# Kernel tuning notes

Hardware: AMD Instinct MI355X
Metric: run time of the kernel (lower is better)

## Reference

```python
import jax, jax.numpy as jnp
import numpy as np

N_NODES = 100000
N_EDGES = 1600000
EMBED_DIM = 64


def setup_inputs() -> dict:
    key = jax.random.key(0)
    k1, k2, k3, k4 = jax.random.split(key, 4)
    ego_embeddings = jax.random.normal(k1, (N_NODES, EMBED_DIM), dtype=jnp.float32)
    adj_values = jax.random.uniform(k2, (N_EDGES,), dtype=jnp.float32)
    adj_rows = jax.random.randint(k3, (N_EDGES,), 0, N_NODES, dtype=jnp.int32)
    adj_cols = jax.random.randint(k4, (N_EDGES,), 0, N_NODES, dtype=jnp.int32)
    return {
        "ego_embeddings": ego_embeddings,
        "adj_values": adj_values,
        "adj_rows": adj_rows,
        "adj_cols": adj_cols,
    }


def reference(ego_embeddings, adj_values, adj_rows, adj_cols):
    # out[r, :] = sum_{e : rows[e]==r} values[e] * ego_embeddings[cols[e], :]
    # == tf.sparse.sparse_dense_matmul(adj, ego_embeddings)
    messages = adj_values[:, None] * ego_embeddings[adj_cols]  # [E, D]
    out = jax.ops.segment_sum(messages, adj_rows, num_segments=N_NODES)  # [N, D]
    return out
```

## Files before the change

### kernel.cpp

```cpp
#include <hip/hip_runtime.h>

#define N_NODES 100000
#define N_EDGES 1600000
#define EMBED_DIM 64

#define RPB 128
#define NBKT ((N_NODES + RPB - 1) / RPB)
#define CAP 2304
#define TILE 4096
#define NTILE ((N_EDGES + TILE - 1) / TILE)
#define OVCAP 8192
#define EPT 3

__global__ __launch_bounds__(1024) void k_binA(const int* __restrict__ rows,
                                               const int* __restrict__ cols,
                                               const float* __restrict__ vals,
                                               int* __restrict__ gcur,
                                               int2* __restrict__ packed,
                                               int* __restrict__ ov_cnt,
                                               int4* __restrict__ ov) {
    __shared__ int hist[NBKT];
    __shared__ int off[NBKT];
    __shared__ int cur[NBKT];
    __shared__ int gbase[NBKT];
    __shared__ int wsum[16];
    __shared__ int stotal;
    __shared__ int2 stage[TILE];
    __shared__ int dg[TILE];
    const int tid = threadIdx.x;
    const int lane = tid & 63;
    const int wid = tid >> 6;
    const int e0 = blockIdx.x * TILE;

    for (int i = tid; i < NBKT; i += 1024) hist[i] = 0;
    __syncthreads();

    const int eb = e0 + 4 * tid;
    int rr0 = -1, rr1 = -1, rr2 = -1, rr3 = -1;
    if (eb + 3 < N_EDGES) {
        int4 r4 = *(const int4*)(rows + eb);
        rr0 = r4.x; rr1 = r4.y; rr2 = r4.z; rr3 = r4.w;
    } else {
        if (eb + 0 < N_EDGES) rr0 = rows[eb + 0];
        if (eb + 1 < N_EDGES) rr1 = rows[eb + 1];
        if (eb + 2 < N_EDGES) rr2 = rows[eb + 2];
        if (eb + 3 < N_EDGES) rr3 = rows[eb + 3];
    }
    if (rr0 >= 0) atomicAdd(&hist[rr0 >> 7], 1);
    if (rr1 >= 0) atomicAdd(&hist[rr1 >> 7], 1);
    if (rr2 >= 0) atomicAdd(&hist[rr2 >> 7], 1);
    if (rr3 >= 0) atomicAdd(&hist[rr3 >> 7], 1);
    __syncthreads();

    int v = (tid < NBKT) ? hist[tid] : 0;
    int incl = v;
    for (int o = 1; o < 64; o <<= 1) {
        int t = __shfl_up(incl, o, 64);
        if (lane >= o) incl += t;
    }
    if (lane == 63) wsum[wid] = incl;
    __syncthreads();
    if (wid == 0 && lane < 16) {
        int s = wsum[lane];
        int si = s;
        for (int o = 1; o < 16; o <<= 1) {
            int t = __shfl_up(si, o, 64);
            if (lane >= o) si += t;
        }
        wsum[lane] = si - s;
        if (lane == 15) stotal = si;
    }
    __syncthreads();
    int excl = incl - v + wsum[wid];
    if (tid < NBKT) { off[tid] = excl; cur[tid] = excl; }

    for (int b = tid; b < NBKT; b += 1024) {
        int c = hist[b];
        gbase[b] = c ? atomicAdd(&gcur[b], c) : 0;
    }
    __syncthreads();

    int cc0 = 0, cc1 = 0, cc2 = 0, cc3 = 0;
    float vv0 = 0.f, vv1 = 0.f, vv2 = 0.f, vv3 = 0.f;
    if (eb + 3 < N_EDGES) {
        int4 c4 = *(const int4*)(cols + eb);
        float4 v4 = *(const float4*)(vals + eb);
        cc0 = c4.x; cc1 = c4.y; cc2 = c4.z; cc3 = c4.w;
        vv0 = v4.x; vv1 = v4.y; vv2 = v4.z; vv3 = v4.w;
    } else {
        if (eb + 0 < N_EDGES) { cc0 = cols[eb + 0]; vv0 = vals[eb + 0]; }
        if (eb + 1 < N_EDGES) { cc1 = cols[eb + 1]; vv1 = vals[eb + 1]; }
        if (eb + 2 < N_EDGES) { cc2 = cols[eb + 2]; vv2 = vals[eb + 2]; }
        if (eb + 3 < N_EDGES) { cc3 = cols[eb + 3]; vv3 = vals[eb + 3]; }
    }
#define PLACE(RR, CC, VV)                                                     \
    if (RR >= 0) {                                                            \
        int b_ = RR >> 7;                                                     \
        int p_ = atomicAdd(&cur[b_], 1);                                      \
        stage[p_] = make_int2(((RR & (RPB - 1)) << 17) | CC,                  \
                              __float_as_int(VV));                            \
        int d_ = gbase[b_] + (p_ - off[b_]);                                  \
        dg[p_] = (d_ < CAP) ? (b_ * CAP + d_) : (0x40000000 | b_);            \
    }
    PLACE(rr0, cc0, vv0)
    PLACE(rr1, cc1, vv1)
    PLACE(rr2, cc2, vv2)
    PLACE(rr3, cc3, vv3)
#undef PLACE
    __syncthreads();

    int total = stotal;
    for (int j = tid; j < total; j += 1024) {
        int d = dg[j];
        int2 ev = stage[j];
        if (d & 0x40000000) {
            int b_ = d & 0xFFFF;
            int ovi = atomicAdd(ov_cnt, 1);
            if (ovi < OVCAP) {
                int r = b_ * RPB + (((unsigned)ev.x) >> 17);
                ov[ovi] = make_int4(r, ev.x & 0x1FFFF, ev.y, 0);
            }
        } else {
            packed[d] = ev;
        }
    }
}

__global__ __launch_bounds__(1024) void k_bg(const float* __restrict__ x,
                                             const int* __restrict__ gcur,
                                             const int2* __restrict__ packed,
                                             const int* __restrict__ ov_cnt,
                                             const int4* __restrict__ ov,
                                             float* __restrict__ out) {
    __shared__ int2 stage[CAP];
    __shared__ int h[RPB];
    __shared__ int ofs[RPB];
    __shared__ int cur[RPB];
    __shared__ int wsum[2];
    const int b = blockIdx.x;
    const int tid = threadIdx.x;
    const int lane = tid & 63;
    const int wid = tid >> 6;
    int n = gcur[b];
    if (n > CAP) n = CAP;
    const int base = b * CAP;

    if (tid < RPB) h[tid] = 0;
    __syncthreads();

    int2 ereg[EPT];
    int lr[EPT];
#pragma unroll
    for (int jj = 0; jj < EPT; ++jj) {
        int j = tid + jj * 1024;
        lr[jj] = -1;
        if (j < n) {
            int2 e = packed[base + j];
            ereg[jj] = e;
            int r = ((unsigned)e.x) >> 17;
            lr[jj] = r;
            atomicAdd(&h[r], 1);
        }
    }
    __syncthreads();

    int hv = (tid < RPB) ? h[tid] : 0;
    int incl = hv;
    for (int o = 1; o < 64; o <<= 1) {
        int t = __shfl_up(incl, o, 64);
        if (lane >= o) incl += t;
    }
    if (tid < RPB && lane == 63) wsum[wid] = incl;
    __syncthreads();
    if (wid == 0 && lane < 2) {
        int s = wsum[lane];
        int si = s;
        {
            int t = __shfl_up(si, 1, 64);
            if (lane >= 1) si += t;
        }
        wsum[lane] = si - s;
    }
    __syncthreads();
    if (tid < RPB) {
        int o2 = incl - hv + wsum[wid];
        ofs[tid] = o2;
        cur[tid] = o2;
    }
    __syncthreads();

#pragma unroll
    for (int jj = 0; jj < EPT; ++jj) {
        if (lr[jj] >= 0) {
            int p = atomicAdd(&cur[lr[jj]], 1);
            stage[p] = ereg[jj];
        }
    }
    __syncthreads();

    const int half = lane >> 5;
    const int hl = lane & 31;
    const float2* __restrict__ x2 = (const float2*)x;
    for (int i = 0; i < 8; ++i) {
        int r = wid * 8 + i;
        int grow = b * RPB + r;
        if (grow >= N_NODES) break;
        int deg = h[r];
        int beg = ofs[r];
        float ax = 0.f, ay = 0.f;
        for (int j0 = 0; j0 < deg; j0 += 16) {
            float pv[8];
            float2 xv[8];
#pragma unroll
            for (int k = 0; k < 8; ++k) {
                int j = j0 + 2 * k + half;
                int2 e = (j < deg) ? stage[beg + j] : make_int2(0, 0);
                pv[k] = __int_as_float(e.y);
                xv[k] = x2[(e.x & 0x1FFFF) * 32 + hl];
            }
#pragma unroll
            for (int k = 0; k < 8; ++k) {
                ax += pv[k] * xv[k].x;
                ay += pv[k] * xv[k].y;
            }
        }
        ax += __shfl_xor(ax, 32);
        ay += __shfl_xor(ay, 32);
        if (half == 0) {
            ((float2*)out)[(size_t)grow * 32 + hl] = make_float2(ax, ay);
        }
    }

    __syncthreads();
    int nov = *ov_cnt;
    if (nov > OVCAP) nov = OVCAP;
    for (int i = wid; i < nov; i += 16) {
        int4 e = ov[i];
        if ((e.x >> 7) == b) {
            atomicAdd(&out[(size_t)e.x * EMBED_DIM + lane],
                      __int_as_float(e.z) * x[(size_t)e.y * EMBED_DIM + lane]);
        }
    }
}

__global__ __launch_bounds__(256) void spmm_scatter_kernel(
    const float* __restrict__ x, const float* __restrict__ vals,
    const int* __restrict__ rows, const int* __restrict__ cols,
    float* __restrict__ out) {
    const int wave_in_block = threadIdx.x >> 6;
    const int lane = threadIdx.x & 63;
    const int e = blockIdx.x * 4 + wave_in_block;
    if (e >= N_EDGES) return;
    const float m = vals[e] * x[cols[e] * EMBED_DIM + lane];
    atomicAdd(&out[rows[e] * EMBED_DIM + lane], m);
}

extern "C" void kernel_launch(void* const* d_in, const int* in_sizes, int n_in,
                              void* d_out, int out_size, void* d_ws, size_t ws_size,
                              hipStream_t stream) {
    const float* x    = (const float*)d_in[0];
    const float* vals = (const float*)d_in[1];
    const int*   rows = (const int*)d_in[2];
    const int*   cols = (const int*)d_in[3];
    float* out = (float*)d_out;

    const size_t packed_b = (size_t)NBKT * CAP * 8;
    const size_t ov_b     = (size_t)OVCAP * 16;
    const size_t need = packed_b + ov_b + ((size_t)NBKT + 1) * 4;
    if (ws_size < need) {
        hipMemsetAsync(out, 0, (size_t)out_size * sizeof(float), stream);
        spmm_scatter_kernel<<<(N_EDGES + 3) / 4, 256, 0, stream>>>(x, vals, rows, cols, out);
        return;
    }

    int2* packed  = (int2*)d_ws;
    int4* ov      = (int4*)((char*)d_ws + packed_b);
    int*  gcur    = (int*)((char*)d_ws + packed_b + ov_b);
    int*  ov_cnt  = gcur + NBKT;

    hipMemsetAsync(gcur, 0, ((size_t)NBKT + 1) * sizeof(int), stream);

    k_binA<<<NTILE, 1024, 0, stream>>>(rows, cols, vals, gcur, packed, ov_cnt, ov);
    k_bg<<<NBKT, 1024, 0, stream>>>(x, gcur, (const int2*)packed, ov_cnt, ov, out);
}
```

Measured before the change: 165.8 us.

## Replace global bucket atomics with per-tile sorted segments gathered by consumer

The binning kernel no longer reserves global slots per bucket with atomics. Each tile now writes its locally bucket-sorted edges contiguously, plus a per-tile offset table. The gather kernel scans each bucket's segment lengths across all tiles and copies those segments into shared memory, spilling overflow to a small shared list. This removes the global atomics, the memset and the scattered global writes, at the cost of serial per-tile segment copies by up to 391 threads and a second random-ish read pattern. It also drops the global overflow buffer scan that every block used to do.

```diff
diff --git a/kernel.cpp b/kernel.cpp
--- a/kernel.cpp
+++ b/kernel.cpp
@@ -6,45 +6,47 @@
 
 #define RPB 128
 #define NBKT ((N_NODES + RPB - 1) / RPB)
-#define CAP 2304
 #define TILE 4096
 #define NTILE ((N_EDGES + TILE - 1) / TILE)
-#define OVCAP 8192
+#define OFFW (NBKT + 1)
+#define SCAP 2816
 #define EPT 3
 
 __global__ __launch_bounds__(1024) void k_binA(const int* __restrict__ rows,
                                                const int* __restrict__ cols,
                                                const float* __restrict__ vals,
-                                               int* __restrict__ gcur,
-                                               int2* __restrict__ packed,
-                                               int* __restrict__ ov_cnt,
-                                               int4* __restrict__ ov) {
+                                               int* __restrict__ off_g,
+                                               int2* __restrict__ packed2) {
     __shared__ int hist[NBKT];
-    __shared__ int off[NBKT];
     __shared__ int cur[NBKT];
-    __shared__ int gbase[NBKT];
     __shared__ int wsum[16];
-    __shared__ int stotal;
     __shared__ int2 stage[TILE];
-    __shared__ int dg[TILE];
     const int tid = threadIdx.x;
     const int lane = tid & 63;
     const int wid = tid >> 6;
-    const int e0 = blockIdx.x * TILE;
+    const int blk = blockIdx.x;
+    const int e0 = blk * TILE;
+    const int total = (blk == NTILE - 1) ? (N_EDGES - e0) : TILE;
 
     for (int i = tid; i < NBKT; i += 1024) hist[i] = 0;
     __syncthreads();
 
     const int eb = e0 + 4 * tid;
     int rr0 = -1, rr1 = -1, rr2 = -1, rr3 = -1;
+    int cc0 = 0, cc1 = 0, cc2 = 0, cc3 = 0;
+    float vv0 = 0.f, vv1 = 0.f, vv2 = 0.f, vv3 = 0.f;
     if (eb + 3 < N_EDGES) {
         int4 r4 = *(const int4*)(rows + eb);
+        int4 c4 = *(const int4*)(cols + eb);
+        float4 v4 = *(const float4*)(vals + eb);
         rr0 = r4.x; rr1 = r4.y; rr2 = r4.z; rr3 = r4.w;
+        cc0 = c4.x; cc1 = c4.y; cc2 = c4.z; cc3 = c4.w;
+        vv0 = v4.x; vv1 = v4.y; vv2 = v4.z; vv3 = v4.w;
     } else {
-        if (eb + 0 < N_EDGES) rr0 = rows[eb + 0];
-        if (eb + 1 < N_EDGES) rr1 = rows[eb + 1];
-        if (eb + 2 < N_EDGES) rr2 = rows[eb + 2];
-        if (eb + 3 < N_EDGES) rr3 = rows[eb + 3];
+        if (eb + 0 < N_EDGES) { rr0 = rows[eb + 0]; cc0 = cols[eb + 0]; vv0 = vals[eb + 0]; }
+        if (eb + 1 < N_EDGES) { rr1 = rows[eb + 1]; cc1 = cols[eb + 1]; vv1 = vals[eb + 1]; }
+        if (eb + 2 < N_EDGES) { rr2 = rows[eb + 2]; cc2 = cols[eb + 2]; vv2 = vals[eb + 2]; }
+        if (eb + 3 < N_EDGES) { rr3 = rows[eb + 3]; cc3 = cols[eb + 3]; vv3 = vals[eb + 3]; }
     }
     if (rr0 >= 0) atomicAdd(&hist[rr0 >> 7], 1);
     if (rr1 >= 0) atomicAdd(&hist[rr1 >> 7], 1);
@@ -68,39 +70,21 @@
             if (lane >= o) si += t;
         }
         wsum[lane] = si - s;
-        if (lane == 15) stotal = si;
     }
     __syncthreads();
     int excl = incl - v + wsum[wid];
-    if (tid < NBKT) { off[tid] = excl; cur[tid] = excl; }
-
-    for (int b = tid; b < NBKT; b += 1024) {
-        int c = hist[b];
-        gbase[b] = c ? atomicAdd(&gcur[b], c) : 0;
-    }
-    __syncthreads();
-
-    int cc0 = 0, cc1 = 0, cc2 = 0, cc3 = 0;
-    float vv0 = 0.f, vv1 = 0.f, vv2 = 0.f, vv3 = 0.f;
-    if (eb + 3 < N_EDGES) {
-        int4 c4 = *(const int4*)(cols + eb);
-        float4 v4 = *(const float4*)(vals + eb);
-        cc0 = c4.x; cc1 = c4.y; cc2 = c4.z; cc3 = c4.w;
-        vv0 = v4.x; vv1 = v4.y; vv2 = v4.z; vv3 = v4.w;
-    } else {
-        if (eb + 0 < N_EDGES) { cc0 = cols[eb + 0]; vv0 = vals[eb + 0]; }
-        if (eb + 1 < N_EDGES) { cc1 = cols[eb + 1]; vv1 = vals[eb + 1]; }
-        if (eb + 2 < N_EDGES) { cc2 = cols[eb + 2]; vv2 = vals[eb + 2]; }
-        if (eb + 3 < N_EDGES) { cc3 = cols[eb + 3]; vv3 = vals[eb + 3]; }
-    }
+    if (tid < NBKT) {
+        cur[tid] = excl;
+        off_g[blk * OFFW + tid] = excl;
+    }
+    if (tid == 0) off_g[blk * OFFW + NBKT] = total;
+    __syncthreads();
+
 #define PLACE(RR, CC, VV)                                                     \
     if (RR >= 0) {                                                            \
-        int b_ = RR >> 7;                                                     \
-        int p_ = atomicAdd(&cur[b_], 1);                                      \
+        int p_ = atomicAdd(&cur[RR >> 7], 1);                                 \
         stage[p_] = make_int2(((RR & (RPB - 1)) << 17) | CC,                  \
                               __float_as_int(VV));                            \
-        int d_ = gbase[b_] + (p_ - off[b_]);                                  \
-        dg[p_] = (d_ < CAP) ? (b_ * CAP + d_) : (0x40000000 | b_);            \
     }
     PLACE(rr0, cc0, vv0)
     PLACE(rr1, cc1, vv1)
@@ -109,44 +93,78 @@
 #undef PLACE
     __syncthreads();
 
-    int total = stotal;
-    for (int j = tid; j < total; j += 1024) {
-        int d = dg[j];
-        int2 ev = stage[j];
-        if (d & 0x40000000) {
-            int b_ = d & 0xFFFF;
-            int ovi = atomicAdd(ov_cnt, 1);
-            if (ovi < OVCAP) {
-                int r = b_ * RPB + (((unsigned)ev.x) >> 17);
-                ov[ovi] = make_int4(r, ev.x & 0x1FFFF, ev.y, 0);
-            }
-        } else {
-            packed[d] = ev;
-        }
-    }
+    int4* dst4 = (int4*)(packed2 + e0);
+    const int4* src4 = (const int4*)stage;
+    for (int j = tid; j < total / 2; j += 1024) dst4[j] = src4[j];
 }
 
 __global__ __launch_bounds__(1024) void k_bg(const float* __restrict__ x,
-                                             const int* __restrict__ gcur,
-                                             const int2* __restrict__ packed,
-                                             const int* __restrict__ ov_cnt,
-                                             const int4* __restrict__ ov,
+                                             const int* __restrict__ off_g,
+                                             const int2* __restrict__ packed2,
                                              float* __restrict__ out) {
-    __shared__ int2 stage[CAP];
+    __shared__ int2 stage[SCAP];
     __shared__ int h[RPB];
     __shared__ int ofs[RPB];
     __shared__ int cur[RPB];
-    __shared__ int wsum[2];
+    __shared__ int wsum[16];
+    __shared__ int sdst[NTILE];
+    __shared__ int sbeg[NTILE];
+    __shared__ int2 ovl[64];
+    __shared__ int ovn, sn;
     const int b = blockIdx.x;
     const int tid = threadIdx.x;
     const int lane = tid & 63;
     const int wid = tid >> 6;
-    int n = gcur[b];
-    if (n > CAP) n = CAP;
-    const int base = b * CAP;
 
     if (tid < RPB) h[tid] = 0;
-    __syncthreads();
+    if (tid == 0) ovn = 0;
+
+    int len = 0, s = 0;
+    if (tid < NTILE) {
+        s = off_g[tid * OFFW + b];
+        int e_ = off_g[tid * OFFW + b + 1];
+        len = e_ - s;
+    }
+    int incl = len;
+    for (int o = 1; o < 64; o <<= 1) {
+        int t = __shfl_up(incl, o, 64);
+        if (lane >= o) incl += t;
+    }
+    if (lane == 63) wsum[wid] = incl;
+    __syncthreads();
+    if (wid == 0 && lane < 16) {
+        int s2 = wsum[lane];
+        int si = s2;
+        for (int o = 1; o < 16; o <<= 1) {
+            int t = __shfl_up(si, o, 64);
+            if (lane >= o) si += t;
+        }
+        wsum[lane] = si - s2;
+    }
+    __syncthreads();
+    int dst = incl - len + wsum[wid];
+    if (tid == 1023) sn = dst;
+    if (tid < NTILE) { sdst[tid] = dst; sbeg[tid] = tid * TILE + s; }
+    __syncthreads();
+
+    if (tid < NTILE) {
+        int sb = sbeg[tid];
+        for (int k = 0; k < len; ++k) {
+            int2 e = packed2[sb + k];
+            int idx = dst + k;
+            if (idx < SCAP) {
+                stage[idx] = e;
+                atomicAdd(&h[((unsigned)e.x) >> 17], 1);
+            } else {
+                int oi = atomicAdd(&ovn, 1);
+                if (oi < 64) ovl[oi] = e;
+            }
+        }
+    }
+    __syncthreads();
+
+    int n = sn;
+    if (n > SCAP) n = SCAP;
 
     int2 ereg[EPT];
     int lr[EPT];
@@ -155,35 +173,32 @@
         int j = tid + jj * 1024;
         lr[jj] = -1;
         if (j < n) {
-            int2 e = packed[base + j];
+            int2 e = stage[j];
             ereg[jj] = e;
-            int r = ((unsigned)e.x) >> 17;
-            lr[jj] = r;
-            atomicAdd(&h[r], 1);
-        }
-    }
-    __syncthreads();
+            lr[jj] = ((unsigned)e.x) >> 17;
+        }
+    }
 
     int hv = (tid < RPB) ? h[tid] : 0;
-    int incl = hv;
+    int hin = hv;
     for (int o = 1; o < 64; o <<= 1) {
-        int t = __shfl_up(incl, o, 64);
-        if (lane >= o) incl += t;
-    }
-    if (tid < RPB && lane == 63) wsum[wid] = incl;
+        int t = __shfl_up(hin, o, 64);
+        if (lane >= o) hin += t;
+    }
+    if (tid < RPB && lane == 63) wsum[wid] = hin;
     __syncthreads();
     if (wid == 0 && lane < 2) {
-        int s = wsum[lane];
-        int si = s;
+        int s2 = wsum[lane];
+        int si = s2;
         {
             int t = __shfl_up(si, 1, 64);
             if (lane >= 1) si += t;
         }
-        wsum[lane] = si - s;
+        wsum[lane] = si - s2;
     }
     __syncthreads();
     if (tid < RPB) {
-        int o2 = incl - hv + wsum[wid];
+        int o2 = hin - hv + wsum[wid];
         ofs[tid] = o2;
         cur[tid] = o2;
     }
@@ -232,13 +247,15 @@
     }
 
     __syncthreads();
-    int nov = *ov_cnt;
-    if (nov > OVCAP) nov = OVCAP;
-    for (int i = wid; i < nov; i += 16) {
-        int4 e = ov[i];
-        if ((e.x >> 7) == b) {
-            atomicAdd(&out[(size_t)e.x * EMBED_DIM + lane],
-                      __int_as_float(e.z) * x[(size_t)e.y * EMBED_DIM + lane]);
+    if (wid == 0) {
+        int nov = ovn;
+        if (nov > 64) nov = 64;
+        for (int i = 0; i < nov; ++i) {
+            int2 e = ovl[i];
+            int r = b * RPB + (((unsigned)e.x) >> 17);
+            int c = e.x & 0x1FFFF;
+            atomicAdd(&out[(size_t)r * EMBED_DIM + lane],
+                      __int_as_float(e.y) * x[(size_t)c * EMBED_DIM + lane]);
         }
     }
 }
@@ -264,22 +281,18 @@
     const int*   cols = (const int*)d_in[3];
     float* out = (float*)d_out;
 
-    const size_t packed_b = (size_t)NBKT * CAP * 8;
-    const size_t ov_b     = (size_t)OVCAP * 16;
-    const size_t need = packed_b + ov_b + ((size_t)NBKT + 1) * 4;
+    const size_t packed_b = (size_t)NTILE * TILE * 8;
+    const size_t off_b    = (size_t)NTILE * OFFW * 4;
+    const size_t need = packed_b + off_b;
     if (ws_size < need) {
         hipMemsetAsync(out, 0, (size_t)out_size * sizeof(float), stream);
         spmm_scatter_kernel<<<(N_EDGES + 3) / 4, 256, 0, stream>>>(x, vals, rows, cols, out);
         return;
     }
 
-    int2* packed  = (int2*)d_ws;
-    int4* ov      = (int4*)((char*)d_ws + packed_b);
-    int*  gcur    = (int*)((char*)d_ws + packed_b + ov_b);
-    int*  ov_cnt  = gcur + NBKT;
-
-    hipMemsetAsync(gcur, 0, ((size_t)NBKT + 1) * sizeof(int), stream);
-
-    k_binA<<<NTILE, 1024, 0, stream>>>(rows, cols, vals, gcur, packed, ov_cnt, ov);
-    k_bg<<<NBKT, 1024, 0, stream>>>(x, gcur, (const int2*)packed, ov_cnt, ov, out);
-}
+    int2* packed2 = (int2*)d_ws;
+    int*  off_g   = (int*)((char*)d_ws + packed_b);
+
+    k_binA<<<NTILE, 1024, 0, stream>>>(rows, cols, vals, off_g, packed2);
+    k_bg<<<NBKT, 1024, 0, stream>>>(x, off_g, (const int2*)packed2, out);
+}
```

New measurement: 168.9 us. Within noise of the previous version (+1.8%).
